# Kernel tuning notes

Measured on AMD Instinct MI355X. Metric: run time of the kernel, lower is better.

## Reference

```python
import jax, jax.numpy as jnp
import numpy as np

N = 50000
E = 800000
D = 128


def setup_inputs() -> dict:
    key = jax.random.key(0)
    ks = jax.random.split(key, 6)
    x = jax.random.normal(ks[0], (N, D), dtype=jnp.float32)
    W_self = jax.random.normal(ks[1], (D, D), dtype=jnp.float32) * (1.0 / np.sqrt(D))
    b_self = jax.random.normal(ks[2], (D,), dtype=jnp.float32) * 0.01
    W_neigh = jax.random.normal(ks[3], (D, D), dtype=jnp.float32) * (1.0 / np.sqrt(D))
    src = jax.random.randint(ks[4], (E,), 0, N, dtype=jnp.int32)
    dst = jax.random.randint(ks[5], (E,), 0, N, dtype=jnp.int32)
    # Row-normalized adjacency: weight of edge (src -> dst) is 1/deg(dst)
    deg = jax.ops.segment_sum(jnp.ones((E,), jnp.float32), dst, num_segments=N)
    edge_w = 1.0 / jnp.maximum(deg, 1.0)[dst]
    return {"x": x, "W_self": W_self, "b_self": b_self, "W_neigh": W_neigh,
            "edge_w": edge_w, "src": src, "dst": dst}


def reference(x, W_self, b_self, W_neigh, edge_w, src, dst):
    n = x.shape[0]
    # neigh = A @ x  (row-normalized sparse adjacency as weighted edge list)
    msgs = x[src] * edge_w[:, None]               # (E, D) gather + scale
    neigh = jax.ops.segment_sum(msgs, dst, num_segments=n)  # (N, D) scatter-add
    # lin_self(x) + lin_neigh(neigh)  (torch Linear: y = x @ W.T + b)
    return x @ W_self.T + b_self + neigh @ W_neigh.T
```

## Files before the change

### kernel.cpp

```cpp
#include <hip/hip_runtime.h>
#include <hip/hip_bf16.h>

#define N_NODES 50000
#define N_EDGES 800000
#define DIM 128

#define RSH 6
#define RNODES 64
#define NRANGE 782
#define CH 4096
#define NB 196
#define NTOT (NRANGE * NB)
#define NSCANB ((NTOT + 1023) / 1024)
#define BCAP 64
#define MM_BLOCKS ((N_NODES + 63) / 64)

typedef __attribute__((ext_vector_type(8))) short bf16x8;
typedef __attribute__((ext_vector_type(4))) float f32x4;

union BU8 { uint4 u; bf16x8 b; };

static __device__ __forceinline__ ushort f2bf(float f) {
    __hip_bfloat16 h = __float2bfloat16(f);
    return *reinterpret_cast<ushort*>(&h);
}
static __device__ __forceinline__ uint pack2(float a, float b) {
    return (uint)f2bf(a) | ((uint)f2bf(b) << 16);
}
static __device__ __forceinline__ float bflo(uint u) { return __uint_as_float(u << 16); }
static __device__ __forceinline__ float bfhi(uint u) { return __uint_as_float(u & 0xffff0000u); }

__global__ __launch_bounds__(256) void hist_k(const int* __restrict__ dst,
                                              int* __restrict__ histg,
                                              int* __restrict__ ovfcnt) {
    __shared__ int h[NRANGE];
    int t = threadIdx.x, b = blockIdx.x;
    if (b == 0 && t == 0) *ovfcnt = 0;
    for (int i = t; i < NRANGE; i += 256) h[i] = 0;
    __syncthreads();
    int e0 = b * CH;
    int n = N_EDGES - e0; if (n > CH) n = CH;
    for (int i = t; i < n; i += 256) atomicAdd(&h[dst[e0 + i] >> RSH], 1);
    __syncthreads();
    for (int i = t; i < NRANGE; i += 256) histg[b * NRANGE + i] = h[i];
}

__global__ __launch_bounds__(1024) void scanA_k(const int* __restrict__ histg,
                                                int* __restrict__ off,
                                                int* __restrict__ bsum) {
    __shared__ int lds[1024];
    int t = threadIdx.x;
    int c = blockIdx.x * 1024 + t;
    int v = 0;
    if (c < NTOT) {
        int r = c / NB, b = c - r * NB;
        v = histg[b * NRANGE + r];
    }
    lds[t] = v;
    __syncthreads();
    for (int s = 1; s < 1024; s <<= 1) {
        int add = (t >= s) ? lds[t - s] : 0;
        __syncthreads();
        lds[t] += add;
        __syncthreads();
    }
    if (c < NTOT) off[c] = lds[t] - v;
    if (t == 1023) bsum[blockIdx.x] = lds[1023];
}

__global__ __launch_bounds__(256, 4) void mmscat_k(const float* __restrict__ x,
                                                   const float* __restrict__ Ws,
                                                   const float* __restrict__ Wn,
                                                   const float* __restrict__ bias,
                                                   const int* __restrict__ src,
                                                   const int* __restrict__ dst,
                                                   const int* __restrict__ off,
                                                   const int* __restrict__ bsum,
                                                   float* __restrict__ out,
                                                   ushort* __restrict__ Yn,
                                                   uint* __restrict__ buf) {
    __shared__ ushort wlds[16384];
    int tid = threadIdx.x;

    if (blockIdx.x >= MM_BLOCKS) {
        int b = blockIdx.x - MM_BLOCKS;
        int* cur = (int*)wlds;
        int* sb  = (int*)wlds + NRANGE;

        int v = (tid < NSCANB) ? bsum[tid] : 0;
        sb[tid] = v;
        __syncthreads();
        for (int s = 1; s < 256; s <<= 1) {
            int add = (tid >= s) ? sb[tid - s] : 0;
            __syncthreads();
            sb[tid] += add;
            __syncthreads();
        }
        sb[tid] -= v;
        __syncthreads();

        for (int i = tid; i < NRANGE; i += 256) {
            int c = i * NB + b;
            cur[i] = off[c] + sb[c >> 10];
        }
        __syncthreads();

        int e0 = b * CH;
        int n = N_EDGES - e0; if (n > CH) n = CH;
        for (int i = tid; i < n; i += 256) {
            int e = e0 + i;
            int d = dst[e];
            int r = d >> RSH;
            int pos = atomicAdd(&cur[r], 1);
            buf[pos] = ((uint)src[e] << RSH) | (uint)(d & (RNODES - 1));
        }
        return;
    }

    int lane = tid & 63;
    int w    = tid >> 6;
    int lr   = lane & 15;
    int g    = lane >> 4;
    int myrow0 = blockIdx.x * 64 + w * 16;

    bf16x8 a[4];
    {
        int row = myrow0 + lr;
        bool ok = row < N_NODES;
        const float* ap = x + (size_t)row * 128;
#pragma unroll
        for (int kf = 0; kf < 4; ++kf) {
            float4 f0 = make_float4(0.f, 0.f, 0.f, 0.f), f1 = f0;
            if (ok) {
                f0 = *(const float4*)(ap + kf * 32 + g * 8);
                f1 = *(const float4*)(ap + kf * 32 + g * 8 + 4);
            }
            BU8 u;
            u.u.x = pack2(f0.x, f0.y); u.u.y = pack2(f0.z, f0.w);
            u.u.z = pack2(f1.x, f1.y); u.u.w = pack2(f1.z, f1.w);
            a[kf] = u.b;
        }
    }

    f32x4 accA[8], accB[8];
#pragma unroll
    for (int nt = 0; nt < 8; ++nt) {
        accA[nt] = (f32x4){0.f, 0.f, 0.f, 0.f};
        accB[nt] = (f32x4){0.f, 0.f, 0.f, 0.f};
    }

    __syncthreads();
#pragma unroll
    for (int i = 0; i < 8; ++i) {
        int f = i * 256 + tid;
        int r = f >> 4, c = f & 15;
        const float* wsrc = Ws + (size_t)r * 128 + c * 8;
        float4 f0 = *(const float4*)(wsrc);
        float4 f1 = *(const float4*)(wsrc + 4);
        uint4 u;
        u.x = pack2(f0.x, f0.y); u.y = pack2(f0.z, f0.w);
        u.z = pack2(f1.x, f1.y); u.w = pack2(f1.z, f1.w);
        *(uint4*)(&wlds[r * 128 + ((c ^ (r & 7)) * 8)]) = u;
    }
    __syncthreads();
#pragma unroll
    for (int nt = 0; nt < 8; ++nt) {
        int row = nt * 16 + lr;
#pragma unroll
        for (int kf = 0; kf < 4; ++kf) {
            int chunk = kf * 4 + g;
            bf16x8 b = *(const bf16x8*)(&wlds[row * 128 + ((chunk ^ (lr & 7)) * 8)]);
            accA[nt] = __builtin_amdgcn_mfma_f32_16x16x32_bf16(a[kf], b, accA[nt], 0, 0, 0);
        }
    }

    __syncthreads();
#pragma unroll
    for (int i = 0; i < 8; ++i) {
        int f = i * 256 + tid;
        int r = f >> 4, c = f & 15;
        const float* wsrc = Wn + (size_t)r * 128 + c * 8;
        float4 f0 = *(const float4*)(wsrc);
        float4 f1 = *(const float4*)(wsrc + 4);
        uint4 u;
        u.x = pack2(f0.x, f0.y); u.y = pack2(f0.z, f0.w);
        u.z = pack2(f1.x, f1.y); u.w = pack2(f1.z, f1.w);
        *(uint4*)(&wlds[r * 128 + ((c ^ (r & 7)) * 8)]) = u;
    }
    __syncthreads();
#pragma unroll
    for (int nt = 0; nt < 8; ++nt) {
        int row = nt * 16 + lr;
#pragma unroll
        for (int kf = 0; kf < 4; ++kf) {
            int chunk = kf * 4 + g;
            bf16x8 b = *(const bf16x8*)(&wlds[row * 128 + ((chunk ^ (lr & 7)) * 8)]);
            accB[nt] = __builtin_amdgcn_mfma_f32_16x16x32_bf16(a[kf], b, accB[nt], 0, 0, 0);
        }
    }

    __syncthreads();
    float* myslice = (float*)wlds + w * 2048;

#pragma unroll
    for (int nt = 0; nt < 8; ++nt) {
        float bv = bias[nt * 16 + lr];
#pragma unroll
        for (int j = 0; j < 4; ++j)
            myslice[(g * 4 + j) * 128 + nt * 16 + lr] = accA[nt][j] + bv;
    }
#pragma unroll
    for (int i = 0; i < 8; ++i) {
        int flat = i * 256 + lane * 4;
        int row = flat >> 7, col = flat & 127;
        int grow = myrow0 + row;
        float4 v = *(float4*)(myslice + flat);
        if (grow < N_NODES) *(float4*)(out + (size_t)grow * 128 + col) = v;
    }

#pragma unroll
    for (int nt = 0; nt < 8; ++nt)
#pragma unroll
        for (int j = 0; j < 4; ++j)
            myslice[(g * 4 + j) * 128 + nt * 16 + lr] = accB[nt][j];
#pragma unroll
    for (int i = 0; i < 4; ++i) {
        int flat = i * 512 + lane * 8;
        int row = flat >> 7, col = flat & 127;
        int grow = myrow0 + row;
        float4 v0 = *(float4*)(myslice + flat);
        float4 v1 = *(float4*)(myslice + flat + 4);
        uint4 u;
        u.x = pack2(v0.x, v0.y); u.y = pack2(v0.z, v0.w);
        u.z = pack2(v1.x, v1.y); u.w = pack2(v1.z, v1.w);
        if (grow < N_NODES) *(uint4*)(Yn + (size_t)grow * 128 + col) = u;
    }
}

__global__ __launch_bounds__(512) void agg4_k(const ushort* __restrict__ Yn,
                                              const uint* __restrict__ buf,
                                              const int* __restrict__ off,
                                              const int* __restrict__ bsum,
                                              float* __restrict__ out,
                                              int* __restrict__ count,
                                              int* __restrict__ ovfcnt,
                                              int2* __restrict__ ovf) {
    __shared__ ushort bkt[RNODES][BCAP];
    __shared__ int cnt[RNODES];
    __shared__ int sb[256];
    int r = blockIdx.x;
    int t = threadIdx.x;
    if (t < RNODES) cnt[t] = 0;

    int v = 0;
    if (t < 256) {
        v = (t < NSCANB) ? bsum[t] : 0;
        sb[t] = v;
    }
    __syncthreads();
    for (int s = 1; s < 256; s <<= 1) {
        int add = 0;
        if (t < 256 && t >= s) add = sb[t - s];
        __syncthreads();
        if (t < 256) sb[t] += add;
        __syncthreads();
    }
    if (t < 256) sb[t] -= v;
    __syncthreads();

    int c0 = r * NB;
    int start = off[c0] + sb[c0 >> 10];
    int end;
    if (r == NRANGE - 1) end = N_EDGES;
    else { int c1 = (r + 1) * NB; end = off[c1] + sb[c1 >> 10]; }

    for (int i = start + t; i < end; i += 512) {
        uint p = buf[i];
        int local = (int)(p & (RNODES - 1));
        int s = (int)(p >> RSH);
        int pos = atomicAdd(&cnt[local], 1);
        if (pos < BCAP) {
            bkt[local][pos] = (ushort)s;
        } else {
            int o = atomicAdd(ovfcnt, 1);
            ovf[o] = make_int2(s, r * RNODES + local);
        }
    }
    __syncthreads();

    int lane = t & 63;
    int wv = t >> 6;
    int g = lane >> 4;
    int c8 = (lane & 15) * 8;

#pragma unroll 1
    for (int q = 0; q < 8; ++q) {
        int n = wv * 8 + q;
        int gnode = r * RNODES + n;
        if (gnode >= N_NODES) continue;
        int deg = cnt[n];
        if (lane == 0) count[gnode] = deg;
        int m = (deg < BCAP) ? deg : BCAP;
        int sreg = (lane < m) ? (int)bkt[n][lane] : 0;

        float acc0 = 0.f, acc1 = 0.f, acc2 = 0.f, acc3 = 0.f;
        float acc4 = 0.f, acc5 = 0.f, acc6 = 0.f, acc7 = 0.f;

#define ACC8(v)                                        \
    do {                                               \
        acc0 += bflo(v.x); acc1 += bfhi(v.x);          \
        acc2 += bflo(v.y); acc3 += bfhi(v.y);          \
        acc4 += bflo(v.z); acc5 += bfhi(v.z);          \
        acc6 += bflo(v.w); acc7 += bfhi(v.w);          \
    } while (0)

        int j = 0;
        for (; j + 8 <= m; j += 8) {
            int s0 = __shfl(sreg, j + g);
            int s1 = __shfl(sreg, j + 4 + g);
            uint4 v0 = *(const uint4*)(Yn + (size_t)s0 * 128 + c8);
            uint4 v1 = *(const uint4*)(Yn + (size_t)s1 * 128 + c8);
            ACC8(v0);
            ACC8(v1);
        }
        for (; j + 4 <= m; j += 4) {
            int s = __shfl(sreg, j + g);
            uint4 vv = *(const uint4*)(Yn + (size_t)s * 128 + c8);
            ACC8(vv);
        }
        if (j < m) {
            int jj = j + g;
            bool valid = jj < m;
            int s = __shfl(sreg, valid ? jj : j);
            uint4 vv = *(const uint4*)(Yn + (size_t)s * 128 + c8);
            if (valid) ACC8(vv);
        }
#undef ACC8

#define RED(a) do { a += __shfl_xor(a, 16); a += __shfl_xor(a, 32); } while (0)
        RED(acc0); RED(acc1); RED(acc2); RED(acc3);
        RED(acc4); RED(acc5); RED(acc6); RED(acc7);
#undef RED

        if (lane < 16) {
            float scale = 1.0f / (float)(deg > 0 ? deg : 1);
            float* orow = out + (size_t)gnode * 128 + c8;
            float4 o0 = *(const float4*)(orow);
            float4 o1 = *(const float4*)(orow + 4);
            o0.x += scale * acc0; o0.y += scale * acc1;
            o0.z += scale * acc2; o0.w += scale * acc3;
            o1.x += scale * acc4; o1.y += scale * acc5;
            o1.z += scale * acc6; o1.w += scale * acc7;
            *(float4*)(orow) = o0;
            *(float4*)(orow + 4) = o1;
        }
    }
}

__global__ void ovf_k(const ushort* __restrict__ Yn, const int* __restrict__ count,
                      const int* __restrict__ ovfcnt, const int2* __restrict__ ovf,
                      float* __restrict__ out) {
    int n = *ovfcnt;
    for (int i = blockIdx.x; i < n; i += gridDim.x) {
        int2 e = ovf[i];
        int s = e.x, d = e.y;
        float scale = 1.0f / (float)max(count[d], 1);
        int c = threadIdx.x;
        float v = __uint_as_float(((uint)Yn[(size_t)s * 128 + c]) << 16);
        atomicAdd(&out[(size_t)d * 128 + c], scale * v);
    }
}

extern "C" void kernel_launch(void* const* d_in, const int* in_sizes, int n_in,
                              void* d_out, int out_size, void* d_ws, size_t ws_size,
                              hipStream_t stream) {
    const float* x       = (const float*)d_in[0];
    const float* W_self  = (const float*)d_in[1];
    const float* b_self  = (const float*)d_in[2];
    const float* W_neigh = (const float*)d_in[3];
    const int* src = (const int*)d_in[5];
    const int* dst = (const int*)d_in[6];
    float* out = (float*)d_out;

    char* ws = (char*)d_ws;
    ushort* Yn     = (ushort*)(ws);
    int*    histg  = (int*)(ws + 12800000);
    int*    off    = (int*)(ws + 13413088);
    uint*   buf    = (uint*)(ws + 14026176);
    int*    count  = (int*)(ws + 17226176);
    int*    ovfcnt = (int*)(ws + 17426176);
    int*    bsum   = (int*)(ws + 17426192);
    int2*   ovf    = (int2*)(ws + 17427216);

    hist_k<<<NB, 256, 0, stream>>>(dst, histg, ovfcnt);
    scanA_k<<<NSCANB, 1024, 0, stream>>>(histg, off, bsum);

    mmscat_k<<<MM_BLOCKS + NB, 256, 0, stream>>>(x, W_self, W_neigh, b_self,
                                                 src, dst, off, bsum,
                                                 out, Yn, buf);

    agg4_k<<<NRANGE, 512, 0, stream>>>(Yn, buf, off, bsum, out, count, ovfcnt, ovf);

    ovf_k<<<64, 128, 0, stream>>>(Yn, count, ovfcnt, ovf, out);
}
```

Measured before the change: 75.05 us.

## Handle high-degree nodes inside aggregation and drop overflow kernel; halve histogram blocks

Nodes whose in-degree exceeds the shared bucket capacity are now handled inside the aggregation kernel by rescanning the range's edge list, rather than being spilled to a global overflow list that a separate atomic-add kernel processes. This removes one kernel launch, the count array, and global atomics. The histogram/scatter chunk size is also doubled, which halves the number of histogram blocks and shrinks the scan. The rescan path is slow but should rarely run given an average degree of about 16.

```diff
diff --git a/kernel.cpp b/kernel.cpp
--- a/kernel.cpp
+++ b/kernel.cpp
@@ -8,8 +8,8 @@
 #define RSH 6
 #define RNODES 64
 #define NRANGE 782
-#define CH 4096
-#define NB 196
+#define CH 8192
+#define NB 98
 #define NTOT (NRANGE * NB)
 #define NSCANB ((NTOT + 1023) / 1024)
 #define BCAP 64
@@ -31,11 +31,9 @@
 static __device__ __forceinline__ float bfhi(uint u) { return __uint_as_float(u & 0xffff0000u); }
 
 __global__ __launch_bounds__(256) void hist_k(const int* __restrict__ dst,
-                                              int* __restrict__ histg,
-                                              int* __restrict__ ovfcnt) {
+                                              int* __restrict__ histg) {
     __shared__ int h[NRANGE];
     int t = threadIdx.x, b = blockIdx.x;
-    if (b == 0 && t == 0) *ovfcnt = 0;
     for (int i = t; i < NRANGE; i += 256) h[i] = 0;
     __syncthreads();
     int e0 = b * CH;
@@ -241,10 +239,7 @@
                                               const uint* __restrict__ buf,
                                               const int* __restrict__ off,
                                               const int* __restrict__ bsum,
-                                              float* __restrict__ out,
-                                              int* __restrict__ count,
-                                              int* __restrict__ ovfcnt,
-                                              int2* __restrict__ ovf) {
+                                              float* __restrict__ out) {
     __shared__ ushort bkt[RNODES][BCAP];
     __shared__ int cnt[RNODES];
     __shared__ int sb[256];
@@ -279,12 +274,7 @@
         int local = (int)(p & (RNODES - 1));
         int s = (int)(p >> RSH);
         int pos = atomicAdd(&cnt[local], 1);
-        if (pos < BCAP) {
-            bkt[local][pos] = (ushort)s;
-        } else {
-            int o = atomicAdd(ovfcnt, 1);
-            ovf[o] = make_int2(s, r * RNODES + local);
-        }
+        if (pos < BCAP) bkt[local][pos] = (ushort)s;
     }
     __syncthreads();
 
@@ -299,9 +289,6 @@
         int gnode = r * RNODES + n;
         if (gnode >= N_NODES) continue;
         int deg = cnt[n];
-        if (lane == 0) count[gnode] = deg;
-        int m = (deg < BCAP) ? deg : BCAP;
-        int sreg = (lane < m) ? (int)bkt[n][lane] : 0;
 
         float acc0 = 0.f, acc1 = 0.f, acc2 = 0.f, acc3 = 0.f;
         float acc4 = 0.f, acc5 = 0.f, acc6 = 0.f, acc7 = 0.f;
@@ -314,26 +301,42 @@
         acc6 += bflo(v.w); acc7 += bfhi(v.w);          \
     } while (0)
 
-        int j = 0;
-        for (; j + 8 <= m; j += 8) {
-            int s0 = __shfl(sreg, j + g);
-            int s1 = __shfl(sreg, j + 4 + g);
-            uint4 v0 = *(const uint4*)(Yn + (size_t)s0 * 128 + c8);
-            uint4 v1 = *(const uint4*)(Yn + (size_t)s1 * 128 + c8);
-            ACC8(v0);
-            ACC8(v1);
-        }
-        for (; j + 4 <= m; j += 4) {
-            int s = __shfl(sreg, j + g);
-            uint4 vv = *(const uint4*)(Yn + (size_t)s * 128 + c8);
-            ACC8(vv);
-        }
-        if (j < m) {
-            int jj = j + g;
-            bool valid = jj < m;
-            int s = __shfl(sreg, valid ? jj : j);
-            uint4 vv = *(const uint4*)(Yn + (size_t)s * 128 + c8);
-            if (valid) ACC8(vv);
+        if (deg <= BCAP) {
+            int m = deg;
+            int sreg = (lane < m) ? (int)bkt[n][lane] : 0;
+            int j = 0;
+            for (; j + 8 <= m; j += 8) {
+                int s0 = __shfl(sreg, j + g);
+                int s1 = __shfl(sreg, j + 4 + g);
+                uint4 v0 = *(const uint4*)(Yn + (size_t)s0 * 128 + c8);
+                uint4 v1 = *(const uint4*)(Yn + (size_t)s1 * 128 + c8);
+                ACC8(v0);
+                ACC8(v1);
+            }
+            for (; j + 4 <= m; j += 4) {
+                int s = __shfl(sreg, j + g);
+                uint4 vv = *(const uint4*)(Yn + (size_t)s * 128 + c8);
+                ACC8(vv);
+            }
+            if (j < m) {
+                int jj = j + g;
+                bool valid = jj < m;
+                int s = __shfl(sreg, valid ? jj : j);
+                uint4 vv = *(const uint4*)(Yn + (size_t)s * 128 + c8);
+                if (valid) ACC8(vv);
+            }
+        } else {
+            for (int i = start; i < end; i += 4) {
+                int idx = i + g;
+                if (idx < end) {
+                    uint p = buf[idx];
+                    if ((int)(p & (RNODES - 1)) == n) {
+                        int s = (int)(p >> RSH);
+                        uint4 vv = *(const uint4*)(Yn + (size_t)s * 128 + c8);
+                        ACC8(vv);
+                    }
+                }
+            }
         }
 #undef ACC8
 
@@ -357,20 +360,6 @@
     }
 }
 
-__global__ void ovf_k(const ushort* __restrict__ Yn, const int* __restrict__ count,
-                      const int* __restrict__ ovfcnt, const int2* __restrict__ ovf,
-                      float* __restrict__ out) {
-    int n = *ovfcnt;
-    for (int i = blockIdx.x; i < n; i += gridDim.x) {
-        int2 e = ovf[i];
-        int s = e.x, d = e.y;
-        float scale = 1.0f / (float)max(count[d], 1);
-        int c = threadIdx.x;
-        float v = __uint_as_float(((uint)Yn[(size_t)s * 128 + c]) << 16);
-        atomicAdd(&out[(size_t)d * 128 + c], scale * v);
-    }
-}
-
 extern "C" void kernel_launch(void* const* d_in, const int* in_sizes, int n_in,
                               void* d_out, int out_size, void* d_ws, size_t ws_size,
                               hipStream_t stream) {
@@ -385,21 +374,16 @@
     char* ws = (char*)d_ws;
     ushort* Yn     = (ushort*)(ws);
     int*    histg  = (int*)(ws + 12800000);
-    int*    off    = (int*)(ws + 13413088);
-    uint*   buf    = (uint*)(ws + 14026176);
-    int*    count  = (int*)(ws + 17226176);
-    int*    ovfcnt = (int*)(ws + 17426176);
-    int*    bsum   = (int*)(ws + 17426192);
-    int2*   ovf    = (int2*)(ws + 17427216);
-
-    hist_k<<<NB, 256, 0, stream>>>(dst, histg, ovfcnt);
+    int*    off    = (int*)(ws + 13106544);
+    uint*   buf    = (uint*)(ws + 13413088);
+    int*    bsum   = (int*)(ws + 16613088);
+
+    hist_k<<<NB, 256, 0, stream>>>(dst, histg);
     scanA_k<<<NSCANB, 1024, 0, stream>>>(histg, off, bsum);
 
     mmscat_k<<<MM_BLOCKS + NB, 256, 0, stream>>>(x, W_self, W_neigh, b_self,
                                                  src, dst, off, bsum,
                                                  out, Yn, buf);
 
-    agg4_k<<<NRANGE, 512, 0, stream>>>(Yn, buf, off, bsum, out, count, ovfcnt, ovf);
-
-    ovf_k<<<64, 128, 0, stream>>>(Yn, count, ovfcnt, ovf, out);
-}
+    agg4_k<<<NRANGE, 512, 0, stream>>>(Yn, buf, off, bsum, out);
+}
```

New measurement: 83.96 us. 11.9% more time.
